# Optimization experiments

Hardware: AMD Instinct MI355X
Metric: run time of the kernel (lower is better)

Reference implementation:

```python
import jax, jax.numpy as jnp
import numpy as np

# --- config (Qwen3-Next linear attention defaults) ---
B, S, H = 1, 256, 2048
NK, NV, DK, DV, K = 4, 32, 128, 128, 4
KEY_DIM = NK * DK          # 512
VAL_DIM = NV * DV          # 4096
CONV_DIM = 2 * KEY_DIM + VAL_DIM  # 5120
EPS = 1e-6


def setup_inputs() -> dict:
    key = jax.random.key(0)
    ks = jax.random.split(key, 8)
    rn = lambda k, shape, sc: jax.random.normal(k, shape, jnp.float32) * sc
    return {
        "hidden_states": jax.random.normal(ks[0], (B, S, H), jnp.float32),
        "w_qkvz": rn(ks[1], (2 * KEY_DIM + 2 * VAL_DIM, H), 0.02),  # in_proj_qkvz weight
        "w_ba": rn(ks[2], (2 * NV, H), 0.02),                        # in_proj_ba weight
        "w_out": rn(ks[3], (H, VAL_DIM), 0.02),                      # out_proj weight
        "conv_w": rn(ks[4], (CONV_DIM, 1, K), 0.1),                  # depthwise conv weight [C,1,K]
        "dt_bias": jnp.ones((NV,), jnp.float32),
        "A_log": jnp.zeros((NV,), jnp.float32),
        "norm_w": jnp.ones((DV,), jnp.float32),
    }


def reference(hidden_states, w_qkvz, w_ba, w_out, conv_w, dt_bias, A_log, norm_w):
    b, s, _ = hidden_states.shape
    # input projections (Linear without bias: x @ W.T)
    qkvz = hidden_states @ w_qkvz.T                      # [B,S,9216]
    ba = hidden_states @ w_ba.T                          # [B,S,64]
    q, k, v, z = jnp.split(qkvz, [KEY_DIM, 2 * KEY_DIM, 2 * KEY_DIM + VAL_DIM], axis=-1)
    beta, alpha = jnp.split(ba, 2, axis=-1)              # each [B,S,NV]

    # causal depthwise conv over concat(q,k,v), then silu
    qkv = jnp.concatenate([q, k, v], axis=-1).transpose(0, 2, 1)   # [B,C,S]
    qkv = jax.lax.conv_general_dilated(
        qkv, conv_w, window_strides=(1,), padding=[(K - 1, 0)],
        dimension_numbers=("NCH", "OIH", "NCH"), feature_group_count=CONV_DIM)
    qkv = jax.nn.silu(qkv).transpose(0, 2, 1)            # [B,S,C]
    q, k, v = jnp.split(qkv, [KEY_DIM, 2 * KEY_DIM], axis=-1)

    q = q.reshape(b, s, NK, DK)
    k = k.reshape(b, s, NK, DK)
    v = v.reshape(b, s, NV, DV)
    z = z.reshape(b, s, NV, DV)

    # GQA-style head expansion (repeat_interleave)
    ratio = NV // NK
    q = jnp.repeat(q, ratio, axis=2)                     # [B,S,NV,DK]
    k = jnp.repeat(k, ratio, axis=2)

    # NOTE: original computes g = -softplus(-A_log - alpha) but never uses it (dead code).
    beta_g = jax.nn.sigmoid(beta + dt_bias)[..., None]   # [B,S,NV,1]
    q = q * (DK ** -0.5)

    # naive delta-rule: full outer-product tensor + cumsum (memory-bound)
    kv = jnp.einsum("bsnk,bsnv->bsnkv", k, v * beta_g)   # [B,S,NV,DK,DV]
    out = jnp.einsum("bsnk,bsnkv->bsnv", q, jnp.cumsum(kv, axis=1))  # [B,S,NV,DV]

    # gated RMSNorm over head_v_dim in fp32
    of = out.astype(jnp.float32)
    var = jnp.mean(of * of, axis=-1, keepdims=True)
    of = of * jax.lax.rsqrt(var + EPS) * norm_w
    of = of * jax.nn.silu(z.astype(jnp.float32))

    return of.reshape(b, s, VAL_DIM) @ w_out.T           # [B,S,H]
```

## Files before the change

kernel.cpp:

```cpp
#include <hip/hip_runtime.h>
#include <hip/hip_bf16.h>

#define S_LEN   256
#define HID     2048
#define NVH     32
#define KEYDIM  512
#define VALDIM  4096
#define CONVDIM 5120
#define QKVZ_N  9216
#define EPS_F   1e-6f

typedef __attribute__((ext_vector_type(8))) short bf16x8;
typedef __attribute__((ext_vector_type(4))) float f32x4;

__device__ __forceinline__ unsigned short f2bf(float f) {
    union { float f; unsigned int i; } v; v.f = f;
    unsigned int x = v.i;
    return (unsigned short)((x + 0x7FFFu + ((x >> 16) & 1u)) >> 16);
}
__device__ __forceinline__ unsigned int pk2(float x, float y) {
    union { __hip_bfloat162 h; unsigned int u; } c;
    c.h = __float22bfloat162_rn(float2{x, y});
    return c.u;
}
__device__ __forceinline__ float4 asf4(uint4 u) {
    union { uint4 u; float4 f; } c; c.u = u; return c.f;
}
__device__ __forceinline__ uint4 cvt8_pack(float4 a, float4 b) {
    uint4 r;
    r.x = pk2(a.x, a.y); r.y = pk2(a.z, a.w);
    r.z = pk2(b.x, b.y); r.w = pk2(b.z, b.w);
    return r;
}
__device__ __forceinline__ float sigmoidf(float x) { return 1.f / (1.f + __expf(-x)); }

__global__ __launch_bounds__(256, 2)
void gemm_tile(const unsigned short* __restrict__ A, const float* __restrict__ B,
               float* __restrict__ Cpart, int N, int K, int kc) {
    __shared__ __align__(16) unsigned short As[2][128][72];
    __shared__ __align__(16) unsigned short Bs[2][128][72];

    const int tid  = threadIdx.x;
    const int lane = tid & 63, wave = tid >> 6;
    const int wm = wave >> 1, wn = wave & 1;
    const int quad = lane >> 4, l16 = lane & 15;
    const int m0 = blockIdx.y * 128, n0 = blockIdx.x * 128;
    const int kbeg = blockIdx.z * kc;
    const int niter = kc >> 6;

    const int arow = tid >> 3, acol = (tid & 7) << 3;
    const int brow = tid >> 1, bcol = (tid & 1) << 5;

    f32x4 acc[4][4];
#pragma unroll
    for (int i = 0; i < 4; i++)
#pragma unroll
        for (int j = 0; j < 4; j++) acc[i][j] = (f32x4){0.f, 0.f, 0.f, 0.f};

    uint4 qa[4], qb[8];
    auto ld_tiles = [&](int kk) {
#pragma unroll
        for (int p = 0; p < 4; p++)
            qa[p] = *(const uint4*)(A + (size_t)(m0 + arow + 32 * p) * K + kk + acol);
        const float* b = B + (size_t)(n0 + brow) * K + kk + bcol;
#pragma unroll
        for (int i = 0; i < 8; i++) qb[i] = *(const uint4*)(b + 4 * i);
    };
    auto st_tiles = [&](int buf) {
#pragma unroll
        for (int p = 0; p < 4; p++)
            *(uint4*)(&As[buf][arow + 32 * p][acol]) = qa[p];
#pragma unroll
        for (int i = 0; i < 4; i++)
            *(uint4*)(&Bs[buf][brow][bcol + 8 * i]) = cvt8_pack(asf4(qb[2 * i]), asf4(qb[2 * i + 1]));
    };

    ld_tiles(kbeg);
    st_tiles(0);
    __syncthreads();

    for (int it = 0; it < niter; ++it) {
        const int cur = it & 1;
        if (it + 1 < niter) ld_tiles(kbeg + (it + 1) * 64);

        bf16x8 af[2][4], bfr[2][4];
#pragma unroll
        for (int t = 0; t < 4; t++) {
#pragma unroll
            for (int ks = 0; ks < 2; ks++) {
                af[ks][t]  = *(const bf16x8*)(&As[cur][wm * 64 + t * 16 + l16][ks * 32 + quad * 8]);
                bfr[ks][t] = *(const bf16x8*)(&Bs[cur][wn * 64 + t * 16 + l16][ks * 32 + quad * 8]);
            }
        }
#pragma unroll
        for (int ks = 0; ks < 2; ks++)
#pragma unroll
            for (int i = 0; i < 4; i++)
#pragma unroll
                for (int j = 0; j < 4; j++)
                    acc[i][j] = __builtin_amdgcn_mfma_f32_16x16x32_bf16(af[ks][i], bfr[ks][j], acc[i][j], 0, 0, 0);

        if (it + 1 < niter) {
            st_tiles(cur ^ 1);
            __syncthreads();
        }
    }

    float* C = Cpart + (size_t)blockIdx.z * 256 * N;
#pragma unroll
    for (int i = 0; i < 4; i++)
#pragma unroll
        for (int j = 0; j < 4; j++)
#pragma unroll
            for (int r = 0; r < 4; r++) {
                int row = m0 + wm * 64 + i * 16 + quad * 4 + r;
                int col = n0 + wn * 64 + j * 16 + l16;
                C[(size_t)row * N + col] = acc[i][j][r];
            }
}

template<int P>
__global__ void reduce_sum(const float* __restrict__ part, float* __restrict__ out, int n) {
    int i = (blockIdx.x * 256 + threadIdx.x) * 4;
    if (i >= n) return;
    float4 s = *(const float4*)(part + i);
#pragma unroll
    for (int p = 1; p < P; p++) {
        float4 v = *(const float4*)(part + (size_t)p * n + i);
        s.x += v.x; s.y += v.y; s.z += v.z; s.w += v.w;
    }
    *(float4*)(out + i) = s;
}

__global__ __launch_bounds__(256)
void ba_proj(const float* __restrict__ hs,
             const float* __restrict__ w_ba,
             float* __restrict__ ba,
             unsigned short* __restrict__ hs_bf) {
    int s = blockIdx.x;
    int n = threadIdx.x & 63, seg = threadIdx.x >> 6;
    const float* x = hs + (size_t)s * HID + seg * 512;
    const float* w = w_ba + (size_t)n * HID + seg * 512;
    float acc = 0.f;
#pragma unroll 4
    for (int k = 0; k < 512; k += 4) {
        float4 xv = *(const float4*)(x + k);
        float4 wv = *(const float4*)(w + k);
        acc += xv.x * wv.x + xv.y * wv.y + xv.z * wv.z + xv.w * wv.w;
    }
    __shared__ float parts[4][64];
    parts[seg][n] = acc;
    int c = threadIdx.x * 8;
    float4 h0 = *(const float4*)(hs + (size_t)s * HID + c);
    float4 h1 = *(const float4*)(hs + (size_t)s * HID + c + 4);
    *(uint4*)(hs_bf + (size_t)s * HID + c) = cvt8_pack(h0, h1);
    __syncthreads();
    if (threadIdx.x < 64)
        ba[s * 64 + threadIdx.x] = parts[0][threadIdx.x] + parts[1][threadIdx.x]
                                 + parts[2][threadIdx.x] + parts[3][threadIdx.x];
}

__global__ void conv_red4(const float* __restrict__ part,
                          const float* __restrict__ conv_w,
                          float* __restrict__ out) {
    int idx = blockIdx.x * blockDim.x + threadIdx.x;
    int s = idx / CONVDIM, c = idx % CONVDIM;
    const size_t PSTR = (size_t)S_LEN * QKVZ_N;
    float acc = 0.f;
#pragma unroll
    for (int j = 0; j < 4; j++) {
        int t = s - 3 + j;
        if (t >= 0) {
            const float* p = part + (size_t)t * QKVZ_N + c;
            float q = p[0] + p[PSTR] + p[2 * PSTR] + p[3 * PSTR];
            acc += q * conv_w[c * 4 + j];
        }
    }
    out[idx] = acc * sigmoidf(acc);
}

__global__ __launch_bounds__(256)
void attn_fused(const float* __restrict__ conv, const float* __restrict__ ba,
                const float* __restrict__ dt_bias, const float* __restrict__ part,
                const float* __restrict__ norm_w,
                unsigned short* __restrict__ normed) {
    const int st = blockIdx.x, n = blockIdx.y, hk = n >> 3;
    const int s0 = st * 16;
    __shared__ float Qs[16][132], Ks[16][132], Vs[16][132], Ss[16][17];
    const int tid = threadIdx.x, sy = tid >> 4, dx = tid & 15;

    {
        const float* qp = conv + (size_t)(s0 + sy) * CONVDIM + hk * 128 + dx * 8;
        *(float4*)&Qs[sy][dx * 8]     = *(const float4*)qp;
        *(float4*)&Qs[sy][dx * 8 + 4] = *(const float4*)(qp + 4);
    }
    float acc[8] = {0.f, 0.f, 0.f, 0.f, 0.f, 0.f, 0.f, 0.f};
    const float dtb = dt_bias[n];

    for (int t0 = 0; t0 <= s0; t0 += 16) {
        const float* kp = conv + (size_t)(t0 + sy) * CONVDIM + KEYDIM + hk * 128 + dx * 8;
        const float* vp = conv + (size_t)(t0 + sy) * CONVDIM + 2 * KEYDIM + n * 128 + dx * 8;
        *(float4*)&Ks[sy][dx * 8]     = *(const float4*)kp;
        *(float4*)&Ks[sy][dx * 8 + 4] = *(const float4*)(kp + 4);
        *(float4*)&Vs[sy][dx * 8]     = *(const float4*)vp;
        *(float4*)&Vs[sy][dx * 8 + 4] = *(const float4*)(vp + 4);
        __syncthreads();
        float dot = 0.f;
#pragma unroll 8
        for (int d = 0; d < 128; d += 4) {
            float4 q = *(const float4*)&Qs[sy][d];
            float4 k = *(const float4*)&Ks[dx][d];
            dot += q.x * k.x + q.y * k.y + q.z * k.z + q.w * k.w;
        }
        int t = t0 + dx, s = s0 + sy;
        float bg = sigmoidf(ba[t * 64 + n] + dtb);
        Ss[sy][dx] = (t <= s) ? dot * 0.08838834764831845f * bg : 0.f;
        __syncthreads();
#pragma unroll
        for (int j = 0; j < 16; j++) {
            float sv = Ss[sy][j];
#pragma unroll
            for (int r = 0; r < 8; r++) acc[r] += sv * Vs[j][dx + 16 * r];
        }
        __syncthreads();
    }
    float ss = 0.f;
#pragma unroll
    for (int r = 0; r < 8; r++) ss += acc[r] * acc[r];
#pragma unroll
    for (int m = 1; m < 16; m <<= 1) ss += __shfl_xor(ss, m, 64);
    float inv = rsqrtf(ss * (1.f / 128.f) + EPS_F);
    const size_t PSTR = (size_t)S_LEN * QKVZ_N;
    const float* zb = part + (size_t)(s0 + sy) * QKVZ_N + CONVDIM + n * 128;
    unsigned short* op = normed + ((size_t)(s0 + sy) * NVH + n) * 128;
#pragma unroll
    for (int r = 0; r < 8; r++) {
        int d = dx + 16 * r;
        float z = zb[d] + zb[d + PSTR] + zb[d + 2 * PSTR] + zb[d + 3 * PSTR];
        float val = acc[r] * inv * norm_w[d] * (z * sigmoidf(z));
        op[d] = f2bf(val);
    }
}

extern "C" void kernel_launch(void* const* d_in, const int* in_sizes, int n_in,
                              void* d_out, int out_size, void* d_ws, size_t ws_size,
                              hipStream_t stream) {
    const float* hs      = (const float*)d_in[0];
    const float* w_qkvz  = (const float*)d_in[1];
    const float* w_ba    = (const float*)d_in[2];
    const float* w_out   = (const float*)d_in[3];
    const float* conv_w  = (const float*)d_in[4];
    const float* dt_bias = (const float*)d_in[5];
    const float* norm_w  = (const float*)d_in[7];

    char* ws = (char*)d_ws;
    float* scratch1        = (float*)ws;
    float* conv            = (float*)(ws + 37748736);
    float* ba              = (float*)(ws + 42991616);
    unsigned short* normed = (unsigned short*)(ws + 43057152);
    unsigned short* hs_bf  = (unsigned short*)(ws + 45154304);
    float* scratch2        = (float*)ws;

    ba_proj<<<S_LEN, 256, 0, stream>>>(hs, w_ba, ba, hs_bf);
    gemm_tile<<<dim3(QKVZ_N / 128, 2, 4), 256, 0, stream>>>(hs_bf, w_qkvz, scratch1, QKVZ_N, HID, HID / 4);
    conv_red4<<<(S_LEN * CONVDIM) / 256, 256, 0, stream>>>(scratch1, conv_w, conv);
    attn_fused<<<dim3(16, NVH), 256, 0, stream>>>(conv, ba, dt_bias, scratch1, norm_w, normed);
    gemm_tile<<<dim3(HID / 128, 2, 16), 256, 0, stream>>>(normed, w_out, scratch2, HID, VALDIM, VALDIM / 16);
    reduce_sum<16><<<(S_LEN * HID) / 1024, 256, 0, stream>>>(scratch2, (float*)d_out, S_LEN * HID);
}
```

Baseline: 303.4 us.

## Store split-K GEMM partials as bf16 and single-buffer GEMM LDS tiles

The split-K partial outputs of both GEMMs are now written as bf16 instead of fp32, and the conv, attention z-gate and final reduction kernels read bf16 partials and widen them. This halves the traffic of the large partial buffers. The GEMM also drops LDS double buffering for a single buffer with an extra barrier, and raises the launch-bounds occupancy hint from 2 to 4. In exchange, the output loses precision because partial sums are rounded to bf16 before reduction, and the single buffer adds a synchronization stall per k-step.

```diff
diff --git a/kernel.cpp b/kernel.cpp
--- a/kernel.cpp
+++ b/kernel.cpp
@@ -13,6 +13,9 @@
 typedef __attribute__((ext_vector_type(8))) short bf16x8;
 typedef __attribute__((ext_vector_type(4))) float f32x4;
 
+__device__ __forceinline__ float bf2f(unsigned short u) {
+    union { unsigned int i; float f; } v; v.i = ((unsigned int)u) << 16; return v.f;
+}
 __device__ __forceinline__ unsigned short f2bf(float f) {
     union { float f; unsigned int i; } v; v.f = f;
     unsigned int x = v.i;
@@ -34,11 +37,11 @@
 }
 __device__ __forceinline__ float sigmoidf(float x) { return 1.f / (1.f + __expf(-x)); }
 
-__global__ __launch_bounds__(256, 2)
+__global__ __launch_bounds__(256, 4)
 void gemm_tile(const unsigned short* __restrict__ A, const float* __restrict__ B,
-               float* __restrict__ Cpart, int N, int K, int kc) {
-    __shared__ __align__(16) unsigned short As[2][128][72];
-    __shared__ __align__(16) unsigned short Bs[2][128][72];
+               unsigned short* __restrict__ Cpart, int N, int K, int kc) {
+    __shared__ __align__(16) unsigned short As[128][72];
+    __shared__ __align__(16) unsigned short Bs[128][72];
 
     const int tid  = threadIdx.x;
     const int lane = tid & 63, wave = tid >> 6;
@@ -66,21 +69,20 @@
 #pragma unroll
         for (int i = 0; i < 8; i++) qb[i] = *(const uint4*)(b + 4 * i);
     };
-    auto st_tiles = [&](int buf) {
+    auto st_tiles = [&]() {
 #pragma unroll
         for (int p = 0; p < 4; p++)
-            *(uint4*)(&As[buf][arow + 32 * p][acol]) = qa[p];
+            *(uint4*)(&As[arow + 32 * p][acol]) = qa[p];
 #pragma unroll
         for (int i = 0; i < 4; i++)
-            *(uint4*)(&Bs[buf][brow][bcol + 8 * i]) = cvt8_pack(asf4(qb[2 * i]), asf4(qb[2 * i + 1]));
+            *(uint4*)(&Bs[brow][bcol + 8 * i]) = cvt8_pack(asf4(qb[2 * i]), asf4(qb[2 * i + 1]));
     };
 
     ld_tiles(kbeg);
-    st_tiles(0);
+    st_tiles();
     __syncthreads();
 
     for (int it = 0; it < niter; ++it) {
-        const int cur = it & 1;
         if (it + 1 < niter) ld_tiles(kbeg + (it + 1) * 64);
 
         bf16x8 af[2][4], bfr[2][4];
@@ -88,8 +90,8 @@
         for (int t = 0; t < 4; t++) {
 #pragma unroll
             for (int ks = 0; ks < 2; ks++) {
-                af[ks][t]  = *(const bf16x8*)(&As[cur][wm * 64 + t * 16 + l16][ks * 32 + quad * 8]);
-                bfr[ks][t] = *(const bf16x8*)(&Bs[cur][wn * 64 + t * 16 + l16][ks * 32 + quad * 8]);
+                af[ks][t]  = *(const bf16x8*)(&As[wm * 64 + t * 16 + l16][ks * 32 + quad * 8]);
+                bfr[ks][t] = *(const bf16x8*)(&Bs[wn * 64 + t * 16 + l16][ks * 32 + quad * 8]);
             }
         }
 #pragma unroll
@@ -101,12 +103,13 @@
                     acc[i][j] = __builtin_amdgcn_mfma_f32_16x16x32_bf16(af[ks][i], bfr[ks][j], acc[i][j], 0, 0, 0);
 
         if (it + 1 < niter) {
-            st_tiles(cur ^ 1);
             __syncthreads();
-        }
-    }
-
-    float* C = Cpart + (size_t)blockIdx.z * 256 * N;
+            st_tiles();
+            __syncthreads();
+        }
+    }
+
+    unsigned short* C = Cpart + (size_t)blockIdx.z * 256 * N;
 #pragma unroll
     for (int i = 0; i < 4; i++)
 #pragma unroll
@@ -115,21 +118,24 @@
             for (int r = 0; r < 4; r++) {
                 int row = m0 + wm * 64 + i * 16 + quad * 4 + r;
                 int col = n0 + wn * 64 + j * 16 + l16;
-                C[(size_t)row * N + col] = acc[i][j][r];
+                C[(size_t)row * N + col] = f2bf(acc[i][j][r]);
             }
 }
 
-template<int P>
-__global__ void reduce_sum(const float* __restrict__ part, float* __restrict__ out, int n) {
-    int i = (blockIdx.x * 256 + threadIdx.x) * 4;
+__global__ void reduce_sum16(const unsigned short* __restrict__ part,
+                             float* __restrict__ out, int n) {
+    int i = (blockIdx.x * 256 + threadIdx.x) * 8;
     if (i >= n) return;
-    float4 s = *(const float4*)(part + i);
-#pragma unroll
-    for (int p = 1; p < P; p++) {
-        float4 v = *(const float4*)(part + (size_t)p * n + i);
-        s.x += v.x; s.y += v.y; s.z += v.z; s.w += v.w;
-    }
-    *(float4*)(out + i) = s;
+    float s[8] = {0.f, 0.f, 0.f, 0.f, 0.f, 0.f, 0.f, 0.f};
+#pragma unroll
+    for (int p = 0; p < 16; p++) {
+        uint4 v = *(const uint4*)(part + (size_t)p * n + i);
+        const unsigned short* u = (const unsigned short*)&v;
+#pragma unroll
+        for (int r = 0; r < 8; r++) s[r] += bf2f(u[r]);
+    }
+    *(float4*)(out + i)     = (float4){s[0], s[1], s[2], s[3]};
+    *(float4*)(out + i + 4) = (float4){s[4], s[5], s[6], s[7]};
 }
 
 __global__ __launch_bounds__(256)
@@ -160,7 +166,7 @@
                                  + parts[2][threadIdx.x] + parts[3][threadIdx.x];
 }
 
-__global__ void conv_red4(const float* __restrict__ part,
+__global__ void conv_red4(const unsigned short* __restrict__ part,
                           const float* __restrict__ conv_w,
                           float* __restrict__ out) {
     int idx = blockIdx.x * blockDim.x + threadIdx.x;
@@ -171,8 +177,8 @@
     for (int j = 0; j < 4; j++) {
         int t = s - 3 + j;
         if (t >= 0) {
-            const float* p = part + (size_t)t * QKVZ_N + c;
-            float q = p[0] + p[PSTR] + p[2 * PSTR] + p[3 * PSTR];
+            const unsigned short* p = part + (size_t)t * QKVZ_N + c;
+            float q = bf2f(p[0]) + bf2f(p[PSTR]) + bf2f(p[2 * PSTR]) + bf2f(p[3 * PSTR]);
             acc += q * conv_w[c * 4 + j];
         }
     }
@@ -181,7 +187,7 @@
 
 __global__ __launch_bounds__(256)
 void attn_fused(const float* __restrict__ conv, const float* __restrict__ ba,
-                const float* __restrict__ dt_bias, const float* __restrict__ part,
+                const float* __restrict__ dt_bias, const unsigned short* __restrict__ part,
                 const float* __restrict__ norm_w,
                 unsigned short* __restrict__ normed) {
     const int st = blockIdx.x, n = blockIdx.y, hk = n >> 3;
@@ -231,12 +237,12 @@
     for (int m = 1; m < 16; m <<= 1) ss += __shfl_xor(ss, m, 64);
     float inv = rsqrtf(ss * (1.f / 128.f) + EPS_F);
     const size_t PSTR = (size_t)S_LEN * QKVZ_N;
-    const float* zb = part + (size_t)(s0 + sy) * QKVZ_N + CONVDIM + n * 128;
+    const unsigned short* zb = part + (size_t)(s0 + sy) * QKVZ_N + CONVDIM + n * 128;
     unsigned short* op = normed + ((size_t)(s0 + sy) * NVH + n) * 128;
 #pragma unroll
     for (int r = 0; r < 8; r++) {
         int d = dx + 16 * r;
-        float z = zb[d] + zb[d + PSTR] + zb[d + 2 * PSTR] + zb[d + 3 * PSTR];
+        float z = bf2f(zb[d]) + bf2f(zb[d + PSTR]) + bf2f(zb[d + 2 * PSTR]) + bf2f(zb[d + 3 * PSTR]);
         float val = acc[r] * inv * norm_w[d] * (z * sigmoidf(z));
         op[d] = f2bf(val);
     }
@@ -254,17 +260,17 @@
     const float* norm_w  = (const float*)d_in[7];
 
     char* ws = (char*)d_ws;
-    float* scratch1        = (float*)ws;
-    float* conv            = (float*)(ws + 37748736);
-    float* ba              = (float*)(ws + 42991616);
-    unsigned short* normed = (unsigned short*)(ws + 43057152);
-    unsigned short* hs_bf  = (unsigned short*)(ws + 45154304);
-    float* scratch2        = (float*)ws;
+    unsigned short* scratch1 = (unsigned short*)ws;
+    float* conv              = (float*)(ws + 18874368);
+    float* ba                = (float*)(ws + 24117248);
+    unsigned short* normed   = (unsigned short*)(ws + 24182784);
+    unsigned short* hs_bf    = (unsigned short*)(ws + 26279936);
+    unsigned short* scratch2 = (unsigned short*)ws;
 
     ba_proj<<<S_LEN, 256, 0, stream>>>(hs, w_ba, ba, hs_bf);
     gemm_tile<<<dim3(QKVZ_N / 128, 2, 4), 256, 0, stream>>>(hs_bf, w_qkvz, scratch1, QKVZ_N, HID, HID / 4);
     conv_red4<<<(S_LEN * CONVDIM) / 256, 256, 0, stream>>>(scratch1, conv_w, conv);
     attn_fused<<<dim3(16, NVH), 256, 0, stream>>>(conv, ba, dt_bias, scratch1, norm_w, normed);
     gemm_tile<<<dim3(HID / 128, 2, 16), 256, 0, stream>>>(normed, w_out, scratch2, HID, VALDIM, VALDIM / 16);
-    reduce_sum<16><<<(S_LEN * HID) / 1024, 256, 0, stream>>>(scratch2, (float*)d_out, S_LEN * HID);
-}
+    reduce_sum16<<<(S_LEN * HID) / 2048, 256, 0, stream>>>(scratch2, (float*)d_out, S_LEN * HID);
+}
```

New measurement: 477.1 us. 1.57x slower.
